# Performance work log

Measured on AMD Instinct MI355X. Metric: run time of the kernel, lower is better.

The kernel has to match this reference:

```python
import jax, jax.numpy as jnp
import numpy as np
from jax import lax

E = 4      # n_experts
K = 2      # top_k
D = 1024   # d_model
B, S = 4, 4096


def setup_inputs() -> dict:
    key = jax.random.key(0)
    ks = jax.random.split(key, 9)
    sc = 1.0 / np.sqrt(D)
    x = jax.random.normal(ks[0], (B, S, D), dtype=jnp.float32)
    Wg = jax.random.normal(ks[1], (E, D, D), dtype=jnp.float32) * sc
    bg = jax.random.normal(ks[2], (E, D), dtype=jnp.float32) * sc
    Wv = jax.random.normal(ks[3], (E, D, D), dtype=jnp.float32) * sc
    bv = jax.random.normal(ks[4], (E, D), dtype=jnp.float32) * sc
    Wd = jax.random.normal(ks[5], (E, D, D), dtype=jnp.float32) * sc
    # decay_bias_init = 1.0 (torch init.constant_)
    bd = jnp.ones((E, D), dtype=jnp.float32)
    Wgate = jax.random.normal(ks[7], (E, D), dtype=jnp.float32) * sc
    return {"x": x, "Wg": Wg, "bg": bg, "Wv": Wv, "bv": bv,
            "Wd": Wd, "bd": bd, "Wgate": Wgate}


def reference(x, Wg, bg, Wv, bv, Wd, bd, Wgate):
    # Per-expert projections (torch Linear: y = x @ W.T + b; W is (out,in))
    g = jnp.einsum('bsd,eod->ebso', x, Wg) + bg[:, None, None, :]  # (E,B,S,D)
    v = jnp.einsum('bsd,eod->ebso', x, Wv) + bv[:, None, None, :]
    d = jnp.einsum('bsd,eod->ebso', x, Wd) + bd[:, None, None, :]
    x_scan = jax.nn.sigmoid(g) * jnp.tanh(v)
    a = 0.001 + 0.998 * jax.nn.sigmoid(d)

    # Causal linear RNN: h_t = a_t * h_{t-1} + x_t, vectorized over (E,B,D)
    xs = jnp.moveaxis(x_scan, 2, 0)  # (S,E,B,D)
    as_ = jnp.moveaxis(a, 2, 0)      # (S,E,B,D)

    def step(h, inp):
        a_t, x_t = inp
        h = a_t * h + x_t
        return h, h

    h0 = jnp.zeros((E, B, x.shape[-1]), dtype=x.dtype)
    _, outs = lax.scan(step, h0, (as_, xs))        # (S,E,B,D)
    expert_outs = jnp.transpose(outs, (2, 0, 3, 1))  # (B,S,D,E)

    # Router: top-k experts per token, softmax over selected logits
    gate_logits = jnp.einsum('bsd,ed->bse', x, Wgate)  # (B,S,E)
    top_vals, top_idx = lax.top_k(gate_logits, K)      # (B,S,K)
    weights = jax.nn.softmax(top_vals, axis=-1)        # (B,S,K)

    idx = jnp.broadcast_to(top_idx[:, :, None, :],
                           (x.shape[0], x.shape[1], x.shape[2], K))
    selected = jnp.take_along_axis(expert_outs, idx, axis=-1)  # (B,S,D,K)
    return (selected * weights[:, :, None, :]).sum(axis=-1)
```

## Files before the change

kernel.cpp:

```cpp
#include <hip/hip_runtime.h>

#define E_EXP 4
#define D_MODEL 1024
#define B_BATCH 4
#define S_SEQ 4096
#define NTOK (B_BATCH*S_SEQ)
#define CHUNK 32
#define NCHUNK (S_SEQ/CHUNK)

typedef float f4 __attribute__((ext_vector_type(4)));
typedef float f32x4 __attribute__((ext_vector_type(4)));
typedef short bf16x8 __attribute__((ext_vector_type(8)));

__device__ __forceinline__ unsigned short f2b(float f){
  union{float f;unsigned u;}v; v.f=f;
  unsigned r = v.u + 0x7fffu + ((v.u>>16)&1u);
  return (unsigned short)(r>>16);
}
__device__ __forceinline__ float b2f_lo(unsigned v){ union{unsigned u;float f;}x; x.u=v<<16; return x.f; }
__device__ __forceinline__ float b2f_hi(unsigned v){ union{unsigned u;float f;}x; x.u=v&0xffff0000u; return x.f; }

__device__ __forceinline__ void gload_lds16(const void* g, void* l){
  __builtin_amdgcn_global_load_lds(
      (const __attribute__((address_space(1))) void*)g,
      (__attribute__((address_space(3))) void*)l, 16, 0, 0);
}

__global__ __launch_bounds__(256) void prep(
    const float* __restrict__ x, const float* __restrict__ Wgate,
    unsigned short* __restrict__ xbf, float* __restrict__ wtok)
{
  int tok  = blockIdx.x*4 + (threadIdx.x>>6);
  int lane = threadIdx.x & 63;
  const float* xr = x + (size_t)tok*D_MODEL;
  unsigned short* xb = xbf + (size_t)tok*D_MODEL;
  float acc0=0.f,acc1=0.f,acc2=0.f,acc3=0.f;
  #pragma unroll
  for (int j=0;j<4;j++){
    int k = lane*4 + j*256;
    f4 v  = *(const f4*)(xr + k);
    f4 w0 = *(const f4*)(Wgate + 0*D_MODEL + k);
    f4 w1 = *(const f4*)(Wgate + 1*D_MODEL + k);
    f4 w2 = *(const f4*)(Wgate + 2*D_MODEL + k);
    f4 w3 = *(const f4*)(Wgate + 3*D_MODEL + k);
    #pragma unroll
    for (int q=0;q<4;q++){
      acc0 += v[q]*w0[q];
      acc1 += v[q]*w1[q];
      acc2 += v[q]*w2[q];
      acc3 += v[q]*w3[q];
    }
    ushort4 o; o.x=f2b(v[0]); o.y=f2b(v[1]); o.z=f2b(v[2]); o.w=f2b(v[3]);
    *(ushort4*)(xb + k) = o;
  }
  #pragma unroll
  for (int off=32;off>0;off>>=1){
    acc0 += __shfl_down(acc0,off);
    acc1 += __shfl_down(acc1,off);
    acc2 += __shfl_down(acc2,off);
    acc3 += __shfl_down(acc3,off);
  }
  if (lane==0){
    float l[4]={acc0,acc1,acc2,acc3};
    int i1=0;
    #pragma unroll
    for(int e=1;e<4;e++) if (l[e]>l[i1]) i1=e;
    int i2=-1;
    #pragma unroll
    for(int e=0;e<4;e++){ if(e==i1) continue; if(i2<0||l[e]>l[i2]) i2=e; }
    float ex = __expf(l[i2]-l[i1]);
    float w1 = 1.f/(1.f+ex);
    float w2 = ex/(1.f+ex);
    float w[4]={0.f,0.f,0.f,0.f};
    w[i1]=w1; w[i2]=w2;
    float* wp = wtok + (size_t)tok*E_EXP;
    wp[0]=w[0]; wp[1]=w[1]; wp[2]=w[2]; wp[3]=w[3];
  }
}

__global__ __launch_bounds__(256) void cvt_w3(const float* __restrict__ Wg,
                                              const float* __restrict__ Wv,
                                              const float* __restrict__ Wd,
                                              unsigned short* __restrict__ Wcat,
                                              int e0)
{
  const size_t DD = (size_t)D_MODEL*D_MODEL;
  size_t i4 = ((size_t)blockIdx.x*256 + threadIdx.x)*4;
  size_t le3m = i4 >> 20;
  size_t rem  = i4 & (DD-1);
  int mat = (int)(le3m % 3);
  int le  = (int)(le3m / 3);
  const float* src = (mat==0 ? Wg : (mat==1 ? Wv : Wd)) + (size_t)(e0+le)*DD + rem;
  f4 v = *(const f4*)src;
  ushort4 o; o.x=f2b(v[0]); o.y=f2b(v[1]); o.z=f2b(v[2]); o.w=f2b(v[3]);
  *(ushort4*)(Wcat + le3m*DD + rem) = o;
}

#define BM2 256
#define BN2 256
#define BK2 64
#define NT2 (D_MODEL/BK2)

__global__ __launch_bounds__(512, 2) void gemm256(
    const unsigned short* __restrict__ A,
    const unsigned short* __restrict__ Wcat,
    unsigned short* __restrict__ gvd)
{
  __shared__ unsigned short sA[2][BM2][BK2];
  __shared__ unsigned short sB[2][BN2][BK2];
  const size_t DD = (size_t)D_MODEL*D_MODEL;
  const size_t ND = (size_t)NTOK*D_MODEL;

  const int le    = blockIdx.z;
  const int mbase = blockIdx.x*BM2;
  const int ntile = blockIdx.y;
  const int mat   = ntile>>2;
  const int nbase = (ntile&3)*BN2;

  const int tid  = threadIdx.x;
  const int wave = tid>>6, lane = tid&63;
  const int wm = wave>>2, wn = wave&3;
  const int l15 = lane&15;
  const int l8  = lane>>3;
  const int lc  = (lane&7) ^ l8;

  const unsigned short* Wmat = Wcat + ((size_t)le*3 + mat)*DD;
  const unsigned short* gA = A + (size_t)(mbase + wave*8 + l8)*D_MODEL + lc*8;
  const int bBw = (wave>>1)*64 + (wave&1)*8;
  const unsigned short* gB = Wmat + (size_t)(nbase + bBw + l8)*D_MODEL + lc*8;

  const int arow = wm*128 + l15;
  const int brow = wn*64  + l15;
  const int ach0 = (((lane>>4)    ) ^ (lane&7))*8;
  const int ach1 = (((lane>>4) + 4) ^ (lane&7))*8;

  f32x4 acc[8][4];
  #pragma unroll
  for (int i=0;i<8;i++)
    #pragma unroll
    for (int j=0;j<4;j++) acc[i][j] = 0;

  bf16x8 af[4][2], bfv[2][2];

#define STAGE_A2(slot,t,mh) do{ \
  gload_lds16(gA + (size_t)((mh)*64)*D_MODEL     + (t)*BK2, &sA[slot][(mh)*64 + wave*8][0]); \
  gload_lds16(gA + (size_t)(128+(mh)*64)*D_MODEL + (t)*BK2, &sA[slot][128+(mh)*64 + wave*8][0]); \
}while(0)
#define STAGE_B2(slot,t,nh) do{ \
  gload_lds16(gB + (size_t)((nh)*32)*D_MODEL    + (t)*BK2, &sB[slot][bBw + (nh)*32][0]); \
  gload_lds16(gB + (size_t)((nh)*32+16)*D_MODEL + (t)*BK2, &sB[slot][bBw + (nh)*32 + 16][0]); \
}while(0)
#define LOAD_A2(slot,mh) do{ \
  _Pragma("unroll") for (int _m=0;_m<4;++_m){ \
    af[_m][0] = *(const bf16x8*)&sA[slot][arow + ((mh)*4+_m)*16][ach0]; \
    af[_m][1] = *(const bf16x8*)&sA[slot][arow + ((mh)*4+_m)*16][ach1]; \
  } \
}while(0)
#define LOAD_B2(slot,nh) do{ \
  _Pragma("unroll") for (int _n=0;_n<2;++_n){ \
    bfv[_n][0] = *(const bf16x8*)&sB[slot][brow + ((nh)*2+_n)*16][ach0]; \
    bfv[_n][1] = *(const bf16x8*)&sB[slot][brow + ((nh)*2+_n)*16][ach1]; \
  } \
}while(0)
#define MQ2(mh,nh) do{ \
  _Pragma("unroll") for (int _m=0;_m<4;++_m) \
  _Pragma("unroll") for (int _n=0;_n<2;++_n) \
  _Pragma("unroll") for (int _k=0;_k<2;++_k) \
    acc[(mh)*4+_m][(nh)*2+_n] = __builtin_amdgcn_mfma_f32_16x16x32_bf16( \
        af[_m][_k], bfv[_n][_k], acc[(mh)*4+_m][(nh)*2+_n], 0,0,0); \
}while(0)
#define KC_LGKM0  asm volatile("s_waitcnt lgkmcnt(0)" ::: "memory")
#define KC_LGKM8  asm volatile("s_waitcnt lgkmcnt(8)" ::: "memory")
#define KC_VM4    asm volatile("s_waitcnt vmcnt(4)" ::: "memory")
#define BAR       __builtin_amdgcn_s_barrier()
#define PRIO1     __builtin_amdgcn_s_setprio(1)
#define PRIO0     __builtin_amdgcn_s_setprio(0)

#define WINDOW2(slot,oslot,T1,T2) do{ \
  LOAD_A2(slot,0); LOAD_B2(slot,0); \
  STAGE_A2(oslot,T1,1); STAGE_B2(oslot,T1,0); \
  KC_LGKM8; BAR; KC_LGKM0; \
  PRIO1; MQ2(0,0); PRIO0; BAR; \
  LOAD_B2(slot,1); \
  BAR; KC_LGKM0; \
  PRIO1; MQ2(0,1); PRIO0; BAR; \
  LOAD_A2(slot,1); \
  STAGE_A2(slot,T2,0); \
  BAR; KC_LGKM0; \
  PRIO1; MQ2(1,1); PRIO0; BAR; \
  LOAD_B2(slot,0); \
  STAGE_B2(slot,T2,1); \
  KC_VM4; BAR; KC_LGKM0; \
  PRIO1; MQ2(1,0); PRIO0; BAR; \
}while(0)

  STAGE_A2(0,0,0); STAGE_A2(0,0,1); STAGE_B2(0,0,0); STAGE_B2(0,0,1);
  STAGE_A2(1,1,0); STAGE_B2(1,1,1);
  KC_VM4; BAR;

  for (int tp=0; tp<NT2/2; ++tp){
    int ta = 2*tp+1;
    int tb = 2*tp+2; if (tb>=NT2) tb -= NT2;
    int tc = 2*tp+3; if (tc>=NT2) tc -= NT2;
    WINDOW2(0,1,ta,tb);
    WINDOW2(1,0,tb,tc);
  }

  asm volatile("s_waitcnt vmcnt(0)" ::: "memory");

  unsigned short* outp = gvd + ((size_t)le*3 + mat)*ND;
  const int me = mbase + wm*128;
  const int ne = nbase + wn*64;
  #pragma unroll
  for (int mi=0;mi<8;mi++){
    #pragma unroll
    for (int r=0;r<4;r++){
      int m = me + mi*16 + (lane>>4)*4 + r;
      size_t rowoff = (size_t)m*D_MODEL;
      #pragma unroll
      for (int ni=0;ni<4;ni++){
        int n = ne + ni*16 + l15;
        outp[rowoff+n] = f2b(acc[mi][ni][r]);
      }
    }
  }
}

__global__ __launch_bounds__(512) void scan_pass1(
    unsigned short* __restrict__ gvd,
    const float* __restrict__ bg, const float* __restrict__ bv, const float* __restrict__ bd,
    float* __restrict__ P, float* __restrict__ U, int e0)
{
  const size_t ND = (size_t)NTOK*D_MODEL;
  int blk = blockIdx.x;
  int c  = blk % NCHUNK;
  int b  = (blk / NCHUNK) % B_BATCH;
  int le = blk / (NCHUNK*B_BATCH);
  int d0 = threadIdx.x*2;
  int e  = e0 + le;

  float bg0 = bg[(size_t)e*D_MODEL+d0], bg1 = bg[(size_t)e*D_MODEL+d0+1];
  float bv0 = bv[(size_t)e*D_MODEL+d0], bv1 = bv[(size_t)e*D_MODEL+d0+1];
  float bd0 = bd[(size_t)e*D_MODEL+d0], bd1 = bd[(size_t)e*D_MODEL+d0+1];

  unsigned short* gp = gvd + (size_t)le*3*ND;
  size_t base = (((size_t)b)*S_SEQ + (size_t)c*CHUNK)*D_MODEL + d0;
  float h0=0.f,h1=0.f,p0=1.f,p1=1.f;
  for (int t=0;t<CHUNK;t++){
    unsigned gw = *(const unsigned*)(gp + base);
    unsigned vw = *(const unsigned*)(gp + ND + base);
    unsigned dw = *(const unsigned*)(gp + 2*ND + base);
    float g0 = b2f_lo(gw)+bg0, g1 = b2f_hi(gw)+bg1;
    float v0 = b2f_lo(vw)+bv0, v1 = b2f_hi(vw)+bv1;
    float dd0 = b2f_lo(dw)+bd0, dd1 = b2f_hi(dw)+bd1;
    float x0 = (1.f/(1.f+__expf(-g0))) * (1.f - 2.f/(__expf(2.f*v0)+1.f));
    float x1 = (1.f/(1.f+__expf(-g1))) * (1.f - 2.f/(__expf(2.f*v1)+1.f));
    float a0 = 0.001f + 0.998f/(1.f+__expf(-dd0));
    float a1 = 0.001f + 0.998f/(1.f+__expf(-dd1));
    h0 = a0*h0 + x0; h1 = a1*h1 + x1;
    p0 *= a0; p1 *= a1;
    unsigned xsw = (unsigned)f2b(x0) | ((unsigned)f2b(x1)<<16);
    unsigned aaw = (unsigned)f2b(a0) | ((unsigned)f2b(a1)<<16);
    *(unsigned*)(gp + base)        = xsw;
    *(unsigned*)(gp + 2*ND + base) = aaw;
    base += D_MODEL;
  }
  size_t sidx = (((size_t)(le*B_BATCH + b))*NCHUNK + c)*D_MODEL + d0;
  P[sidx]=p0; P[sidx+1]=p1;
  U[sidx]=h0; U[sidx+1]=h1;
}

__global__ __launch_bounds__(256) void scan_pass2(
    const float* __restrict__ P, const float* __restrict__ U, float* __restrict__ Hinit)
{
  int ch = blockIdx.x*256 + threadIdx.x;
  int d  = ch & (D_MODEL-1);
  int eb = ch >> 10;
  size_t base = (size_t)eb*NCHUNK*D_MODEL + d;
  float H=0.f;
  for (int c=0;c<NCHUNK;c++){
    size_t idx = base + (size_t)c*D_MODEL;
    Hinit[idx] = H;
    H = P[idx]*H + U[idx];
  }
}

template<int G, int FIRST>
__global__ __launch_bounds__(512) void scan_pass3(
    const unsigned short* __restrict__ gvd,
    const float* __restrict__ Hinit, const float* __restrict__ wtok,
    float* __restrict__ out, int e0)
{
  const size_t ND = (size_t)NTOK*D_MODEL;
  int blk = blockIdx.x;
  int c = blk % NCHUNK;
  int b = blk / NCHUNK;
  int d0 = threadIdx.x*2;
  float h[G][2];
  #pragma unroll
  for (int le=0; le<G; le++){
    size_t hi = (((size_t)(le*B_BATCH+b))*NCHUNK + c)*D_MODEL + d0;
    h[le][0]=Hinit[hi]; h[le][1]=Hinit[hi+1];
  }
  int s0 = c*CHUNK;
  for (int t=0;t<CHUNK;t++){
    size_t n = (size_t)b*S_SEQ + s0 + t;
    float o0=0.f, o1=0.f;
    #pragma unroll
    for (int le=0;le<G;le++){
      float w = wtok[n*E_EXP + e0 + le];
      size_t idx = (size_t)le*3*ND + n*D_MODEL + d0;
      unsigned xv = *(const unsigned*)(gvd + idx);
      unsigned av = *(const unsigned*)(gvd + 2*ND + idx);
      h[le][0] = b2f_lo(av)*h[le][0] + b2f_lo(xv);
      h[le][1] = b2f_hi(av)*h[le][1] + b2f_hi(xv);
      o0 += w*h[le][0];
      o1 += w*h[le][1];
    }
    float* op = out + n*D_MODEL + d0;
    if (FIRST){ op[0]=o0;  op[1]=o1;  }
    else      { op[0]+=o0; op[1]+=o1; }
  }
}

extern "C" void kernel_launch(void* const* d_in, const int* in_sizes, int n_in,
                              void* d_out, int out_size, void* d_ws, size_t ws_size,
                              hipStream_t stream)
{
  const float* x     = (const float*)d_in[0];
  const float* Wg    = (const float*)d_in[1];
  const float* bg    = (const float*)d_in[2];
  const float* Wv    = (const float*)d_in[3];
  const float* bv    = (const float*)d_in[4];
  const float* Wd    = (const float*)d_in[5];
  const float* bd    = (const float*)d_in[6];
  const float* Wgate = (const float*)d_in[7];
  float* out = (float*)d_out;

  const size_t DD        = (size_t)D_MODEL*D_MODEL;
  const size_t ND        = (size_t)NTOK*D_MODEL;
  const size_t wtok_b    = (size_t)NTOK*E_EXP*4;
  const size_t xbf_b     = ND*2;
  const size_t w_per_e   = 3*DD*2;
  const size_t gvd_per_e = 3*ND*2;
  const size_t st_per_e  = (size_t)B_BATCH*NCHUNK*D_MODEL*4;

  int G = 1;
  for (int g = 4; g >= 1; g >>= 1){
    size_t need = wtok_b + xbf_b + (size_t)g*(w_per_e + gvd_per_e + 3*st_per_e);
    if (need <= ws_size){ G = g; break; }
  }

  char* wsb = (char*)d_ws;
  size_t off = 0;
  float*          wtok = (float*)(wsb+off);          off += wtok_b;
  unsigned short* xbf  = (unsigned short*)(wsb+off); off += xbf_b;
  unsigned short* Wcat = (unsigned short*)(wsb+off); off += (size_t)G*w_per_e;
  unsigned short* gvd  = (unsigned short*)(wsb+off); off += (size_t)G*gvd_per_e;
  float*          P    = (float*)(wsb+off);          off += (size_t)G*st_per_e;
  float*          U    = (float*)(wsb+off);          off += (size_t)G*st_per_e;
  float*          Hi   = (float*)(wsb+off);

  prep<<<NTOK/4, 256, 0, stream>>>(x, Wgate, xbf, wtok);

  for (int e0=0; e0<E_EXP; e0+=G){
    cvt_w3<<<(unsigned)((size_t)G*3*DD/1024), 256, 0, stream>>>(Wg, Wv, Wd, Wcat, e0);

    dim3 gg(NTOK/BM2, 3*D_MODEL/BN2, G);
    gemm256<<<gg, 512, 0, stream>>>(xbf, Wcat, gvd);

    scan_pass1<<<G*B_BATCH*NCHUNK, 512, 0, stream>>>(gvd, bg, bv, bd, P, U, e0);
    scan_pass2<<<G*B_BATCH*D_MODEL/256, 256, 0, stream>>>(P, U, Hi);
    bool first = (e0 == 0);
    if (G==4)      scan_pass3<4,1><<<B_BATCH*NCHUNK, 512, 0, stream>>>(gvd, Hi, wtok, out, e0);
    else if (G==2){
      if (first) scan_pass3<2,1><<<B_BATCH*NCHUNK, 512, 0, stream>>>(gvd, Hi, wtok, out, e0);
      else       scan_pass3<2,0><<<B_BATCH*NCHUNK, 512, 0, stream>>>(gvd, Hi, wtok, out, e0);
    } else {
      if (first) scan_pass3<1,1><<<B_BATCH*NCHUNK, 512, 0, stream>>>(gvd, Hi, wtok, out, e0);
      else       scan_pass3<1,0><<<B_BATCH*NCHUNK, 512, 0, stream>>>(gvd, Hi, wtok, out, e0);
    }
  }
}
```

Baseline: 804.6 us.

## Recompute activations in scan pass3 instead of writing them back in pass1

Scan pass1 no longer writes the bf16 x_scan and decay values back over the projection buffer. It now only reads g/v/d and produces chunk summaries, and pass3 re-reads the raw projections and recomputes the sigmoid/tanh activations with biases. Both kernels move to 4 elements per thread with vector loads and stores at 256 threads per block. This removes two bf16 write streams in pass1 in exchange for pass3 reading three streams instead of two and doing the transcendental math twice.

After: 879.8 us. 1.09x slower.

```diff
diff --git a/kernel.cpp b/kernel.cpp
--- a/kernel.cpp
+++ b/kernel.cpp
@@ -19,6 +19,9 @@
 }
 __device__ __forceinline__ float b2f_lo(unsigned v){ union{unsigned u;float f;}x; x.u=v<<16; return x.f; }
 __device__ __forceinline__ float b2f_hi(unsigned v){ union{unsigned u;float f;}x; x.u=v&0xffff0000u; return x.f; }
+
+__device__ __forceinline__ float sigm(float z){ return 1.f/(1.f+__expf(-z)); }
+__device__ __forceinline__ float tanh_f(float z){ return 1.f - 2.f/(__expf(2.f*z)+1.f); }
 
 __device__ __forceinline__ void gload_lds16(const void* g, void* l){
   __builtin_amdgcn_global_load_lds(
@@ -226,8 +229,8 @@
   }
 }
 
-__global__ __launch_bounds__(512) void scan_pass1(
-    unsigned short* __restrict__ gvd,
+__global__ __launch_bounds__(256) void scan_pass1(
+    const unsigned short* __restrict__ gvd,
     const float* __restrict__ bg, const float* __restrict__ bv, const float* __restrict__ bd,
     float* __restrict__ P, float* __restrict__ U, int e0)
 {
@@ -236,38 +239,35 @@
   int c  = blk % NCHUNK;
   int b  = (blk / NCHUNK) % B_BATCH;
   int le = blk / (NCHUNK*B_BATCH);
-  int d0 = threadIdx.x*2;
+  int d0 = threadIdx.x*4;
   int e  = e0 + le;
 
-  float bg0 = bg[(size_t)e*D_MODEL+d0], bg1 = bg[(size_t)e*D_MODEL+d0+1];
-  float bv0 = bv[(size_t)e*D_MODEL+d0], bv1 = bv[(size_t)e*D_MODEL+d0+1];
-  float bd0 = bd[(size_t)e*D_MODEL+d0], bd1 = bd[(size_t)e*D_MODEL+d0+1];
-
-  unsigned short* gp = gvd + (size_t)le*3*ND;
+  f4 bgv = *(const f4*)(bg + (size_t)e*D_MODEL + d0);
+  f4 bvv = *(const f4*)(bv + (size_t)e*D_MODEL + d0);
+  f4 bdv = *(const f4*)(bd + (size_t)e*D_MODEL + d0);
+
+  const unsigned short* gp = gvd + (size_t)le*3*ND;
   size_t base = (((size_t)b)*S_SEQ + (size_t)c*CHUNK)*D_MODEL + d0;
-  float h0=0.f,h1=0.f,p0=1.f,p1=1.f;
+  float h[4]={0.f,0.f,0.f,0.f}, p[4]={1.f,1.f,1.f,1.f};
   for (int t=0;t<CHUNK;t++){
-    unsigned gw = *(const unsigned*)(gp + base);
-    unsigned vw = *(const unsigned*)(gp + ND + base);
-    unsigned dw = *(const unsigned*)(gp + 2*ND + base);
-    float g0 = b2f_lo(gw)+bg0, g1 = b2f_hi(gw)+bg1;
-    float v0 = b2f_lo(vw)+bv0, v1 = b2f_hi(vw)+bv1;
-    float dd0 = b2f_lo(dw)+bd0, dd1 = b2f_hi(dw)+bd1;
-    float x0 = (1.f/(1.f+__expf(-g0))) * (1.f - 2.f/(__expf(2.f*v0)+1.f));
-    float x1 = (1.f/(1.f+__expf(-g1))) * (1.f - 2.f/(__expf(2.f*v1)+1.f));
-    float a0 = 0.001f + 0.998f/(1.f+__expf(-dd0));
-    float a1 = 0.001f + 0.998f/(1.f+__expf(-dd1));
-    h0 = a0*h0 + x0; h1 = a1*h1 + x1;
-    p0 *= a0; p1 *= a1;
-    unsigned xsw = (unsigned)f2b(x0) | ((unsigned)f2b(x1)<<16);
-    unsigned aaw = (unsigned)f2b(a0) | ((unsigned)f2b(a1)<<16);
-    *(unsigned*)(gp + base)        = xsw;
-    *(unsigned*)(gp + 2*ND + base) = aaw;
+    uint2 gw = *(const uint2*)(gp + base);
+    uint2 vw = *(const uint2*)(gp + ND + base);
+    uint2 dw = *(const uint2*)(gp + 2*ND + base);
+    float gv[4]={b2f_lo(gw.x),b2f_hi(gw.x),b2f_lo(gw.y),b2f_hi(gw.y)};
+    float vv[4]={b2f_lo(vw.x),b2f_hi(vw.x),b2f_lo(vw.y),b2f_hi(vw.y)};
+    float dv[4]={b2f_lo(dw.x),b2f_hi(dw.x),b2f_lo(dw.y),b2f_hi(dw.y)};
+    #pragma unroll
+    for (int j=0;j<4;j++){
+      float xj = sigm(gv[j]+bgv[j]) * tanh_f(vv[j]+bvv[j]);
+      float aj = 0.001f + 0.998f*sigm(dv[j]+bdv[j]);
+      h[j] = aj*h[j] + xj;
+      p[j] *= aj;
+    }
     base += D_MODEL;
   }
   size_t sidx = (((size_t)(le*B_BATCH + b))*NCHUNK + c)*D_MODEL + d0;
-  P[sidx]=p0; P[sidx+1]=p1;
-  U[sidx]=h0; U[sidx+1]=h1;
+  *(f4*)(P+sidx) = f4{p[0],p[1],p[2],p[3]};
+  *(f4*)(U+sidx) = f4{h[0],h[1],h[2],h[3]};
 }
 
 __global__ __launch_bounds__(256) void scan_pass2(
@@ -286,8 +286,9 @@
 }
 
 template<int G, int FIRST>
-__global__ __launch_bounds__(512) void scan_pass3(
+__global__ __launch_bounds__(256) void scan_pass3(
     const unsigned short* __restrict__ gvd,
+    const float* __restrict__ bg, const float* __restrict__ bv, const float* __restrict__ bd,
     const float* __restrict__ Hinit, const float* __restrict__ wtok,
     float* __restrict__ out, int e0)
 {
@@ -295,31 +296,50 @@
   int blk = blockIdx.x;
   int c = blk % NCHUNK;
   int b = blk / NCHUNK;
-  int d0 = threadIdx.x*2;
-  float h[G][2];
+  int d0 = threadIdx.x*4;
+
+  float h[G][4];
+  f4 bgv[G], bvv[G], bdv[G];
   #pragma unroll
   for (int le=0; le<G; le++){
     size_t hi = (((size_t)(le*B_BATCH+b))*NCHUNK + c)*D_MODEL + d0;
-    h[le][0]=Hinit[hi]; h[le][1]=Hinit[hi+1];
+    f4 hv = *(const f4*)(Hinit + hi);
+    #pragma unroll
+    for (int j=0;j<4;j++) h[le][j] = hv[j];
+    int e = e0 + le;
+    bgv[le] = *(const f4*)(bg + (size_t)e*D_MODEL + d0);
+    bvv[le] = *(const f4*)(bv + (size_t)e*D_MODEL + d0);
+    bdv[le] = *(const f4*)(bd + (size_t)e*D_MODEL + d0);
   }
   int s0 = c*CHUNK;
   for (int t=0;t<CHUNK;t++){
     size_t n = (size_t)b*S_SEQ + s0 + t;
-    float o0=0.f, o1=0.f;
+    float o[4]={0.f,0.f,0.f,0.f};
     #pragma unroll
     for (int le=0;le<G;le++){
       float w = wtok[n*E_EXP + e0 + le];
-      size_t idx = (size_t)le*3*ND + n*D_MODEL + d0;
-      unsigned xv = *(const unsigned*)(gvd + idx);
-      unsigned av = *(const unsigned*)(gvd + 2*ND + idx);
-      h[le][0] = b2f_lo(av)*h[le][0] + b2f_lo(xv);
-      h[le][1] = b2f_hi(av)*h[le][1] + b2f_hi(xv);
-      o0 += w*h[le][0];
-      o1 += w*h[le][1];
-    }
-    float* op = out + n*D_MODEL + d0;
-    if (FIRST){ op[0]=o0;  op[1]=o1;  }
-    else      { op[0]+=o0; op[1]+=o1; }
+      const unsigned short* gp = gvd + (size_t)le*3*ND + n*D_MODEL + d0;
+      uint2 gw = *(const uint2*)(gp);
+      uint2 vw = *(const uint2*)(gp + ND);
+      uint2 dw = *(const uint2*)(gp + 2*ND);
+      float gv[4]={b2f_lo(gw.x),b2f_hi(gw.x),b2f_lo(gw.y),b2f_hi(gw.y)};
+      float vv[4]={b2f_lo(vw.x),b2f_hi(vw.x),b2f_lo(vw.y),b2f_hi(vw.y)};
+      float dv[4]={b2f_lo(dw.x),b2f_hi(dw.x),b2f_lo(dw.y),b2f_hi(dw.y)};
+      #pragma unroll
+      for (int j=0;j<4;j++){
+        float xj = sigm(gv[j]+bgv[le][j]) * tanh_f(vv[j]+bvv[le][j]);
+        float aj = 0.001f + 0.998f*sigm(dv[j]+bdv[le][j]);
+        h[le][j] = aj*h[le][j] + xj;
+        o[j] += w*h[le][j];
+      }
+    }
+    f4* op = (f4*)(out + n*D_MODEL + d0);
+    if (FIRST){
+      *op = f4{o[0],o[1],o[2],o[3]};
+    } else {
+      f4 cur = *op;
+      *op = f4{cur[0]+o[0],cur[1]+o[1],cur[2]+o[2],cur[3]+o[3]};
+    }
   }
 }
 
@@ -369,16 +389,16 @@
     dim3 gg(NTOK/BM2, 3*D_MODEL/BN2, G);
     gemm256<<<gg, 512, 0, stream>>>(xbf, Wcat, gvd);
 
-    scan_pass1<<<G*B_BATCH*NCHUNK, 512, 0, stream>>>(gvd, bg, bv, bd, P, U, e0);
+    scan_pass1<<<G*B_BATCH*NCHUNK, 256, 0, stream>>>(gvd, bg, bv, bd, P, U, e0);
     scan_pass2<<<G*B_BATCH*D_MODEL/256, 256, 0, stream>>>(P, U, Hi);
     bool first = (e0 == 0);
-    if (G==4)      scan_pass3<4,1><<<B_BATCH*NCHUNK, 512, 0, stream>>>(gvd, Hi, wtok, out, e0);
+    if (G==4)      scan_pass3<4,1><<<B_BATCH*NCHUNK, 256, 0, stream>>>(gvd, bg, bv, bd, Hi, wtok, out, e0);
     else if (G==2){
-      if (first) scan_pass3<2,1><<<B_BATCH*NCHUNK, 512, 0, stream>>>(gvd, Hi, wtok, out, e0);
-      else       scan_pass3<2,0><<<B_BATCH*NCHUNK, 512, 0, stream>>>(gvd, Hi, wtok, out, e0);
+      if (first) scan_pass3<2,1><<<B_BATCH*NCHUNK, 256, 0, stream>>>(gvd, bg, bv, bd, Hi, wtok, out, e0);
+      else       scan_pass3<2,0><<<B_BATCH*NCHUNK, 256, 0, stream>>>(gvd, bg, bv, bd, Hi, wtok, out, e0);
     } else {
-      if (first) scan_pass3<1,1><<<B_BATCH*NCHUNK, 512, 0, stream>>>(gvd, Hi, wtok, out, e0);
-      else       scan_pass3<1,0><<<B_BATCH*NCHUNK, 512, 0, stream>>>(gvd, Hi, wtok, out, e0);
-    }
-  }
-}
+      if (first) scan_pass3<1,1><<<B_BATCH*NCHUNK, 256, 0, stream>>>(gvd, bg, bv, bd, Hi, wtok, out, e0);
+      else       scan_pass3<1,0><<<B_BATCH*NCHUNK, 256, 0, stream>>>(gvd, bg, bv, bd, Hi, wtok, out, e0);
+    }
+  }
+}
```

## Fuse decay sigmoid into GEMM epilogue and remap workgroups for XCD locality

Applied to the files above, without the earlier changes.

The decay projection's bias add and scaled sigmoid now run in the GEMM epilogue, so scan_pass1 only reads the finished decay value and no longer writes it back. This removes one bf16 store stream and some transcendental work from the scan pass. The GEMM also remaps its flat workgroup id so that consecutive tiles fall on the same XCD, aiming for better L2 reuse. The remap hardcodes a 64x12 grid and assumes the workgroup count divides by 8.

After: 848.1 us. +5.4%, slower.

```diff
diff --git a/kernel.cpp b/kernel.cpp
--- a/kernel.cpp
+++ b/kernel.cpp
@@ -104,16 +104,25 @@
 __global__ __launch_bounds__(512, 2) void gemm256(
     const unsigned short* __restrict__ A,
     const unsigned short* __restrict__ Wcat,
-    unsigned short* __restrict__ gvd)
+    unsigned short* __restrict__ gvd,
+    const float* __restrict__ bd, int e0)
 {
   __shared__ unsigned short sA[2][BM2][BK2];
   __shared__ unsigned short sB[2][BN2][BK2];
   const size_t DD = (size_t)D_MODEL*D_MODEL;
   const size_t ND = (size_t)NTOK*D_MODEL;
 
-  const int le    = blockIdx.z;
-  const int mbase = blockIdx.x*BM2;
-  const int ntile = blockIdx.y;
+  int orig = blockIdx.x + 64*(blockIdx.y + 12*blockIdx.z);
+  int nwg  = 768*(int)gridDim.z;
+  int nid  = (orig & 7)*(nwg>>3) + (orig>>3);
+  int sx   = nid & 63;
+  int qq   = nid >> 6;
+  int sy   = qq % 12;
+  int sz   = qq / 12;
+
+  const int le    = sz;
+  const int mbase = sx*BM2;
+  const int ntile = sy;
   const int mat   = ntile>>2;
   const int nbase = (ntile&3)*BN2;
 
@@ -211,24 +220,44 @@
   unsigned short* outp = gvd + ((size_t)le*3 + mat)*ND;
   const int me = mbase + wm*128;
   const int ne = nbase + wn*64;
-  #pragma unroll
-  for (int mi=0;mi<8;mi++){
-    #pragma unroll
-    for (int r=0;r<4;r++){
-      int m = me + mi*16 + (lane>>4)*4 + r;
-      size_t rowoff = (size_t)m*D_MODEL;
+  if (mat == 2){
+    float bdv[4];
+    #pragma unroll
+    for (int ni=0;ni<4;ni++) bdv[ni] = bd[(size_t)(e0+le)*D_MODEL + ne + ni*16 + l15];
+    #pragma unroll
+    for (int mi=0;mi<8;mi++){
       #pragma unroll
-      for (int ni=0;ni<4;ni++){
-        int n = ne + ni*16 + l15;
-        outp[rowoff+n] = f2b(acc[mi][ni][r]);
+      for (int r=0;r<4;r++){
+        int m = me + mi*16 + (lane>>4)*4 + r;
+        size_t rowoff = (size_t)m*D_MODEL;
+        #pragma unroll
+        for (int ni=0;ni<4;ni++){
+          int n = ne + ni*16 + l15;
+          float aa = 0.001f + 0.998f/(1.f+__expf(-(acc[mi][ni][r]+bdv[ni])));
+          outp[rowoff+n] = f2b(aa);
+        }
       }
     }
+  } else {
+    #pragma unroll
+    for (int mi=0;mi<8;mi++){
+      #pragma unroll
+      for (int r=0;r<4;r++){
+        int m = me + mi*16 + (lane>>4)*4 + r;
+        size_t rowoff = (size_t)m*D_MODEL;
+        #pragma unroll
+        for (int ni=0;ni<4;ni++){
+          int n = ne + ni*16 + l15;
+          outp[rowoff+n] = f2b(acc[mi][ni][r]);
+        }
+      }
+    }
   }
 }
 
 __global__ __launch_bounds__(512) void scan_pass1(
     unsigned short* __restrict__ gvd,
-    const float* __restrict__ bg, const float* __restrict__ bv, const float* __restrict__ bd,
+    const float* __restrict__ bg, const float* __restrict__ bv,
     float* __restrict__ P, float* __restrict__ U, int e0)
 {
   const size_t ND = (size_t)NTOK*D_MODEL;
@@ -241,7 +270,6 @@
 
   float bg0 = bg[(size_t)e*D_MODEL+d0], bg1 = bg[(size_t)e*D_MODEL+d0+1];
   float bv0 = bv[(size_t)e*D_MODEL+d0], bv1 = bv[(size_t)e*D_MODEL+d0+1];
-  float bd0 = bd[(size_t)e*D_MODEL+d0], bd1 = bd[(size_t)e*D_MODEL+d0+1];
 
   unsigned short* gp = gvd + (size_t)le*3*ND;
   size_t base = (((size_t)b)*S_SEQ + (size_t)c*CHUNK)*D_MODEL + d0;
@@ -249,20 +277,16 @@
   for (int t=0;t<CHUNK;t++){
     unsigned gw = *(const unsigned*)(gp + base);
     unsigned vw = *(const unsigned*)(gp + ND + base);
-    unsigned dw = *(const unsigned*)(gp + 2*ND + base);
+    unsigned aw = *(const unsigned*)(gp + 2*ND + base);
     float g0 = b2f_lo(gw)+bg0, g1 = b2f_hi(gw)+bg1;
     float v0 = b2f_lo(vw)+bv0, v1 = b2f_hi(vw)+bv1;
-    float dd0 = b2f_lo(dw)+bd0, dd1 = b2f_hi(dw)+bd1;
+    float a0 = b2f_lo(aw),     a1 = b2f_hi(aw);
     float x0 = (1.f/(1.f+__expf(-g0))) * (1.f - 2.f/(__expf(2.f*v0)+1.f));
     float x1 = (1.f/(1.f+__expf(-g1))) * (1.f - 2.f/(__expf(2.f*v1)+1.f));
-    float a0 = 0.001f + 0.998f/(1.f+__expf(-dd0));
-    float a1 = 0.001f + 0.998f/(1.f+__expf(-dd1));
     h0 = a0*h0 + x0; h1 = a1*h1 + x1;
     p0 *= a0; p1 *= a1;
     unsigned xsw = (unsigned)f2b(x0) | ((unsigned)f2b(x1)<<16);
-    unsigned aaw = (unsigned)f2b(a0) | ((unsigned)f2b(a1)<<16);
-    *(unsigned*)(gp + base)        = xsw;
-    *(unsigned*)(gp + 2*ND + base) = aaw;
+    *(unsigned*)(gp + base) = xsw;
     base += D_MODEL;
   }
   size_t sidx = (((size_t)(le*B_BATCH + b))*NCHUNK + c)*D_MODEL + d0;
@@ -367,9 +391,9 @@
     cvt_w3<<<(unsigned)((size_t)G*3*DD/1024), 256, 0, stream>>>(Wg, Wv, Wd, Wcat, e0);
 
     dim3 gg(NTOK/BM2, 3*D_MODEL/BN2, G);
-    gemm256<<<gg, 512, 0, stream>>>(xbf, Wcat, gvd);
-
-    scan_pass1<<<G*B_BATCH*NCHUNK, 512, 0, stream>>>(gvd, bg, bv, bd, P, U, e0);
+    gemm256<<<gg, 512, 0, stream>>>(xbf, Wcat, gvd, bd, e0);
+
+    scan_pass1<<<G*B_BATCH*NCHUNK, 512, 0, stream>>>(gvd, bg, bv, P, U, e0);
     scan_pass2<<<G*B_BATCH*D_MODEL/256, 256, 0, stream>>>(P, U, Hi);
     bool first = (e0 == 0);
     if (G==4)      scan_pass3<4,1><<<B_BATCH*NCHUNK, 512, 0, stream>>>(gvd, Hi, wtok, out, e0);
```
